# Optimization experiments

Measured on AMD Instinct MI355X. Metric: run time of the kernel, lower is better.

## Reference

```python
import jax, jax.numpy as jnp
import numpy as np

N = 100000      # nodes
E = 1600000     # edges per adjacency
NFEAT = 128
NHID = 128


def _digcn_conv(x, w, b, src, dst, edge_attr, num_nodes):
    # x @ W, then gather source, scale by edge weight, scatter-add to dst (PyG add-aggr)
    h = x @ w                                   # [N, out]
    msg = edge_attr[:, None] * h[src]           # [E, out]
    out = jax.ops.segment_sum(msg, dst, num_segments=num_nodes)
    return out + b


def _inception(x, ln_w, ln_b, c1_w, c1_b, c2_w, c2_b,
               edge_index, edge_attr, edge_index2, edge_attr2):
    x0 = x @ ln_w + ln_b
    x1 = _digcn_conv(x, c1_w, c1_b, edge_index[0], edge_index[1], edge_attr, x.shape[0])
    x2 = _digcn_conv(x, c2_w, c2_b, edge_index2[0], edge_index2[1], edge_attr2, x.shape[0])
    # eval mode: dropout is identity; the module sums the three branches
    return x0 + x1 + x2


def _mk_params(key, dims):
    ps = {}
    blocks = [("b1", NFEAT, NHID), ("b2", NHID, NHID), ("b3", NHID, NHID)]
    for name, din, dout in blocks:
        for pfx in ("ln", "c1", "c2"):
            key, k1 = jax.random.split(key)
            ps[f"{name}_{pfx}_w"] = jax.random.normal(k1, (din, dout), jnp.float32) * (1.0 / np.sqrt(din))
            ps[f"{name}_{pfx}_b"] = jnp.zeros((dout,), jnp.float32)
    return ps


def setup_inputs() -> dict:
    key = jax.random.key(0)
    ks = jax.random.split(key, 8)
    inp = {
        "x": jax.random.normal(ks[0], (N, NFEAT), jnp.float32),
        "edge_index": jax.random.randint(ks[1], (2, E), 0, N, jnp.int64 if jax.config.jax_enable_x64 else jnp.int32).astype(jnp.int32),
        "edge_attr": jax.random.uniform(ks[2], (E,), jnp.float32),
        "edge_index2": jax.random.randint(ks[3], (2, E), 0, N).astype(jnp.int32),
        "edge_attr2": jax.random.uniform(ks[4], (E,), jnp.float32),
    }
    inp.update(_mk_params(ks[5], None))
    return inp


def reference(x, edge_index, edge_attr, edge_index2, edge_attr2,
              b1_ln_w, b1_ln_b, b1_c1_w, b1_c1_b, b1_c2_w, b1_c2_b,
              b2_ln_w, b2_ln_b, b2_c1_w, b2_c1_b, b2_c2_w, b2_c2_b,
              b3_ln_w, b3_ln_b, b3_c1_w, b3_c1_b, b3_c2_w, b3_c2_b):
    x = _inception(x, b1_ln_w, b1_ln_b, b1_c1_w, b1_c1_b, b1_c2_w, b1_c2_b,
                   edge_index, edge_attr, edge_index2, edge_attr2)
    x = _inception(x, b2_ln_w, b2_ln_b, b2_c1_w, b2_c1_b, b2_c2_w, b2_c2_b,
                   edge_index, edge_attr, edge_index2, edge_attr2)
    x = _inception(x, b3_ln_w, b3_ln_b, b3_c1_w, b3_c1_b, b3_c2_w, b3_c2_b,
                   edge_index, edge_attr, edge_index2, edge_attr2)
    # torch module splits x per-graph via data.batch (data-dependent shapes);
    # we return the full node embedding matrix [N, NHID] instead.
    return x
```

## Files before the change

kernel.cpp:

```cpp
#include <hip/hip_runtime.h>

#define DIM 128
#define CHUNK 8192
#define NBK 256
#define BSHIFT 10

typedef __attribute__((ext_vector_type(8))) short bf16x8;
typedef __attribute__((ext_vector_type(4))) float f32x4;
typedef __attribute__((ext_vector_type(2))) unsigned u32x2;
typedef __attribute__((ext_vector_type(4))) unsigned u32x4;

static __device__ __forceinline__ short f2bf(float f) {
    union { float f; unsigned u; } v; v.f = f;
    unsigned r = (v.u + 0x7FFF + ((v.u >> 16) & 1)) >> 16;
    return (short)r;
}
static __device__ __forceinline__ float asf(unsigned u) {
    union { unsigned u; float f; } v; v.u = u; return v.f;
}
static __device__ __forceinline__ unsigned asu(float f) {
    union { float f; unsigned u; } v; v.f = f; return v.u;
}
static __device__ __forceinline__ unsigned pk2(float a, float b) {
    return (unsigned)(unsigned short)f2bf(a) | ((unsigned)(unsigned short)f2bf(b) << 16);
}

struct WPtrs { const float* w[9]; };
__global__ __launch_bounds__(256) void prep_w_k(WPtrs p, short* __restrict__ wt)
{
    const int g = blockIdx.x * 256 + threadIdx.x;
    if (g >= 3 * 12 * 8 * 64) return;
    const int lane = g & 63;
    const int ct   = (g >> 6) & 7;
    const int rest = g >> 9;
    const int ks   = rest % 12;
    const int layer = rest / 12;
    const int mat   = ks >> 2;
    const int n     = ct * 16 + (lane & 15);
    const int kbase = (ks & 3) * 32 + (lane >> 4) * 8;
    const float* W = p.w[layer * 3 + mat];
    short* dst = wt + (size_t)layer * 49152 + ks * 4096 + ct * 512 + lane * 8;
#pragma unroll
    for (int j = 0; j < 8; ++j) dst[j] = f2bf(W[(size_t)(kbase + j) * DIM + n]);
}

__global__ __launch_bounds__(256) void cast_k(
    const float* __restrict__ X, short* __restrict__ Xb, int n8)
{
    const int i = blockIdx.x * 256 + threadIdx.x;
    if (i >= n8) return;
    const float4* xp = (const float4*)X + (size_t)i * 2;
    const float4 a = xp[0];
    const float4 b = xp[1];
    bf16x8 v;
    v[0] = f2bf(a.x); v[1] = f2bf(a.y); v[2] = f2bf(a.z); v[3] = f2bf(a.w);
    v[4] = f2bf(b.x); v[5] = f2bf(b.y); v[6] = f2bf(b.z); v[7] = f2bf(b.w);
    *(bf16x8*)(Xb + (size_t)i * 8) = v;
}

__global__ __launch_bounds__(256) void mfma_gemm_k(
    const short* __restrict__ Xb, const short* __restrict__ G1,
    const short* __restrict__ G2, const short* __restrict__ Wp,
    const float* __restrict__ b0, const float* __restrict__ b1,
    const float* __restrict__ b2,
    float* __restrict__ Yf, short* __restrict__ Yb, int N)
{
    __shared__ __align__(16) short As[64][384 + 8];
    __shared__ __align__(16) short Bs[4096];
    const int t  = threadIdx.x;
    const int m0 = blockIdx.x * 64;

    for (int idx = t; idx < 64 * 48; idx += 256) {
        const int r = idx / 48;
        const int c = (idx % 48) * 8;
        bf16x8 v = (bf16x8){0,0,0,0,0,0,0,0};
        if (m0 + r < N) {
            if (c < 128)
                v = *(const bf16x8*)(Xb + (size_t)(m0 + r) * DIM + c);
            else if (c < 256)
                v = __builtin_nontemporal_load((const bf16x8*)(G1 + (size_t)(m0 + r) * DIM + (c - 128)));
            else
                v = __builtin_nontemporal_load((const bf16x8*)(G2 + (size_t)(m0 + r) * DIM + (c - 256)));
        }
        *(bf16x8*)&As[r][c] = v;
    }
    __syncthreads();

    const int wave  = t >> 6;
    const int lane  = t & 63;
    const int l15   = lane & 15;
    const int kq    = lane >> 4;
    const int mbase = wave * 16;

    bf16x8 afr[12];
#pragma unroll
    for (int ks = 0; ks < 12; ++ks)
        afr[ks] = *(const bf16x8*)&As[mbase + l15][ks * 32 + kq * 8];

    f32x4 acc[8];
#pragma unroll
    for (int ct = 0; ct < 8; ++ct) acc[ct] = (f32x4){0.f, 0.f, 0.f, 0.f};

#pragma unroll
    for (int ks = 0; ks < 12; ++ks) {
        if (ks) __syncthreads();
        const uint4* wsrc = (const uint4*)(Wp + ks * 4096);
        ((uint4*)Bs)[t]       = wsrc[t];
        ((uint4*)Bs)[t + 256] = wsrc[t + 256];
        __syncthreads();

        const bf16x8 a = afr[ks];
#pragma unroll
        for (int ct = 0; ct < 8; ++ct) {
            const bf16x8 b = *(const bf16x8*)&Bs[ct * 512 + lane * 8];
            acc[ct] = __builtin_amdgcn_mfma_f32_16x16x32_bf16(a, b, acc[ct], 0, 0, 0);
        }
    }

#pragma unroll
    for (int ct = 0; ct < 8; ++ct) {
        const int col = ct * 16 + l15;
        const float bias = b0[col] + b1[col] + b2[col];
#pragma unroll
        for (int r = 0; r < 4; ++r) {
            const int m = m0 + mbase + kq * 4 + r;
            if (m >= N) continue;
            const float v = acc[ct][r] + bias;
            if (Yf) __builtin_nontemporal_store(v, &Yf[(size_t)m * DIM + col]);
            else    Yb[(size_t)m * DIM + col] = f2bf(v);
        }
    }
}


__global__ __launch_bounds__(256) void p0_bhist_k(
    const int* __restrict__ d1, const int* __restrict__ d2,
    int* __restrict__ bcnt, int N, int E, int E2)
{
    __shared__ int lh[NBK];
    const int t = threadIdx.x;
    lh[t] = 0;
    __syncthreads();
    const int stride = gridDim.x * 256;
    for (int i = blockIdx.x * 256 + t; i < E;  i += stride) atomicAdd(&lh[d1[i] >> BSHIFT], 1);
    for (int i = blockIdx.x * 256 + t; i < E2; i += stride) atomicAdd(&lh[(N + d2[i]) >> BSHIFT], 1);
    __syncthreads();
    if (lh[t]) atomicAdd(&bcnt[t], lh[t]);
}

__global__ __launch_bounds__(256) void bscan_k(
    const int* __restrict__ bcnt, int* __restrict__ bktbase,
    int* __restrict__ cursor, int* __restrict__ rowptr, int twoN, int ET)
{
    __shared__ int sv[NBK];
    const int t = threadIdx.x;
    sv[t] = bcnt[t];
    __syncthreads();
    for (int off = 1; off < NBK; off <<= 1) {
        int a = (t >= off) ? sv[t - off] : 0;
        __syncthreads();
        sv[t] += a;
        __syncthreads();
    }
    const int excl = t ? sv[t - 1] : 0;
    bktbase[t] = excl;
    cursor[t]  = excl;
    if (t == 0) rowptr[twoN] = ET;
}

__global__ __launch_bounds__(256) void p1_bin_k(
    const int* __restrict__ s1, const int* __restrict__ d1, const float* __restrict__ ea1,
    const int* __restrict__ s2, const int* __restrict__ d2, const float* __restrict__ ea2,
    int* __restrict__ cursor, uint2* __restrict__ binned,
    int N, int E, int E2, int nc1)
{
    __shared__ __align__(16) uint2 stage[CHUNK];
    __shared__ unsigned char lbkt[CHUNK];
    __shared__ int hist[NBK], exclv[NBK], lcur[NBK], gpos[NBK];

    const int t = threadIdx.x;
    const int c = blockIdx.x;
    const bool a2 = (c >= nc1);
    const int* S  = a2 ? s2  : s1;
    const int* D  = a2 ? d2  : d1;
    const float* W = a2 ? ea2 : ea1;
    const int Eloc = a2 ? E2 : E;
    const int voff = a2 ? N : 0;
    const int eb   = (a2 ? (c - nc1) : c) * CHUNK;
    const int ec   = min(CHUNK, Eloc - eb);

    hist[t] = 0;
    __syncthreads();

    for (int i = t; i < ec; i += 256)
        atomicAdd(&hist[(unsigned)(voff + D[eb + i]) >> BSHIFT], 1);
    __syncthreads();

    exclv[t] = hist[t];
    __syncthreads();
    for (int off = 1; off < NBK; off <<= 1) {
        int a = (t >= off) ? exclv[t - off] : 0;
        __syncthreads();
        exclv[t] += a;
        __syncthreads();
    }
    const int myincl = exclv[t];
    __syncthreads();
    exclv[t] = myincl - hist[t];
    lcur[t]  = exclv[t];
    if (hist[t]) gpos[t] = atomicAdd(&cursor[t], hist[t]);
    __syncthreads();

    for (int i = t; i < ec; i += 256) {
        const int v = voff + D[eb + i];
        const int b = (unsigned)v >> BSHIFT;
        const int lpos = atomicAdd(&lcur[b], 1);
        stage[lpos] = make_uint2((unsigned)S[eb + i] | ((unsigned)(v & 1023) << 17),
                                 asu(W[eb + i]));
        lbkt[lpos] = (unsigned char)b;
    }
    __syncthreads();

    for (int s = t; s < ec; s += 256) {
        const int b = lbkt[s];
        binned[gpos[b] + (s - exclv[b])] = stage[s];
    }
}

__global__ __launch_bounds__(256) void p2_final_k(
    const uint2* __restrict__ binned, const int* __restrict__ bktbase,
    int* __restrict__ rowptr, uint2* __restrict__ pairs, int twoN)
{
    __shared__ int hist[1024], scn[1024], lcur[1024];
    const int t = threadIdx.x;
    const int b = blockIdx.x;
    const int base = bktbase[b];
    const int cnt  = bktbase[b + 1] - base;
    const int vbase = b << BSHIFT;

    for (int i = t; i < 1024; i += 256) hist[i] = 0;
    __syncthreads();

    for (int i = t; i < cnt; i += 256)
        atomicAdd(&hist[binned[base + i].x >> 17], 1);
    __syncthreads();

    for (int i = t; i < 1024; i += 256) scn[i] = hist[i];
    __syncthreads();
    for (int off = 1; off < 1024; off <<= 1) {
        int a0 = (t       >= off) ? scn[t       - off] : 0;
        int a1 = (t + 256 >= off) ? scn[t + 256 - off] : 0;
        int a2 = (t + 512 >= off) ? scn[t + 512 - off] : 0;
        int a3 = (t + 768 >= off) ? scn[t + 768 - off] : 0;
        __syncthreads();
        scn[t] += a0; scn[t + 256] += a1; scn[t + 512] += a2; scn[t + 768] += a3;
        __syncthreads();
    }
    for (int i = t; i < 1024; i += 256) {
        const int excl = scn[i] - hist[i];
        lcur[i] = excl;
        const int v = vbase + i;
        if (v < twoN) rowptr[v] = base + excl;
    }
    __syncthreads();

    for (int i = t; i < cnt; i += 256) {
        const uint2 e = binned[base + i];
        const int vlow = e.x >> 17;
        const int pos = base + atomicAdd(&lcur[vlow], 1);
        pairs[pos] = make_uint2(e.x & 0x1FFFFu, e.y);
    }
}


static __device__ __forceinline__ void bf2acc8(unsigned w, u32x4 h, float* acc)
{
    const float wf = asf(w);
    acc[0] = fmaf(wf, asf(h.x << 16),         acc[0]);
    acc[1] = fmaf(wf, asf(h.x & 0xFFFF0000u), acc[1]);
    acc[2] = fmaf(wf, asf(h.y << 16),         acc[2]);
    acc[3] = fmaf(wf, asf(h.y & 0xFFFF0000u), acc[3]);
    acc[4] = fmaf(wf, asf(h.z << 16),         acc[4]);
    acc[5] = fmaf(wf, asf(h.z & 0xFFFF0000u), acc[5]);
    acc[6] = fmaf(wf, asf(h.w << 16),         acc[6]);
    acc[7] = fmaf(wf, asf(h.w & 0xFFFF0000u), acc[7]);
}

static __device__ __forceinline__ void gacc16(
    const short* __restrict__ H, const uint2* __restrict__ pairs,
    int start, int end, int s, float* acc)
{
    int j = start;
    for (; j + 7 < end; j += 8) {
        u32x2 p[8]; u32x4 h[8];
#pragma unroll
        for (int q = 0; q < 8; ++q)
            p[q] = __builtin_nontemporal_load((const u32x2*)(pairs + j + q));
#pragma unroll
        for (int q = 0; q < 8; ++q)
            h[q] = *(const u32x4*)(H + (size_t)p[q].x * DIM + s * 8);
#pragma unroll
        for (int q = 0; q < 8; ++q) bf2acc8(p[q].y, h[q], acc);
    }
    if (j + 3 < end) {
        u32x2 p[4]; u32x4 h[4];
#pragma unroll
        for (int q = 0; q < 4; ++q)
            p[q] = __builtin_nontemporal_load((const u32x2*)(pairs + j + q));
#pragma unroll
        for (int q = 0; q < 4; ++q)
            h[q] = *(const u32x4*)(H + (size_t)p[q].x * DIM + s * 8);
#pragma unroll
        for (int q = 0; q < 4; ++q) bf2acc8(p[q].y, h[q], acc);
        j += 4;
    }
    for (; j < end; ++j) {
        const u32x2 p = __builtin_nontemporal_load((const u32x2*)(pairs + j));
        const u32x4 h = *(const u32x4*)(H + (size_t)p.x * DIM + s * 8);
        bf2acc8(p.y, h, acc);
    }
}

__global__ __launch_bounds__(256) void gatherX_k(
    const short* __restrict__ Xb,
    const uint2* __restrict__ pairs, const int* __restrict__ rowptr,
    short* __restrict__ G1, short* __restrict__ G2, int N)
{
    const int node = blockIdx.x * 16 + (threadIdx.x >> 4);
    if (node >= N) return;
    const int s = threadIdx.x & 15;

    const int s1 = rowptr[node];
    const int e1 = rowptr[node + 1];
    const int s2 = rowptr[N + node];
    const int e2 = rowptr[N + node + 1];

    float a1[8] = {0.f, 0.f, 0.f, 0.f, 0.f, 0.f, 0.f, 0.f};
    float a2[8] = {0.f, 0.f, 0.f, 0.f, 0.f, 0.f, 0.f, 0.f};
    gacc16(Xb, pairs, s1, e1, s, a1);
    gacc16(Xb, pairs, s2, e2, s, a2);

    const size_t off = (size_t)node * DIM + s * 8;
    u32x4 o1 = (u32x4){pk2(a1[0], a1[1]), pk2(a1[2], a1[3]),
                       pk2(a1[4], a1[5]), pk2(a1[6], a1[7])};
    u32x4 o2 = (u32x4){pk2(a2[0], a2[1]), pk2(a2[2], a2[3]),
                       pk2(a2[4], a2[5]), pk2(a2[6], a2[7])};
    __builtin_nontemporal_store(o1, (u32x4*)(G1 + off));
    __builtin_nontemporal_store(o2, (u32x4*)(G2 + off));
}

extern "C" void kernel_launch(void* const* d_in, const int* in_sizes, int n_in,
                              void* d_out, int out_size, void* d_ws, size_t ws_size,
                              hipStream_t stream)
{
    const float* x   = (const float*)d_in[0];
    const int*   ei  = (const int*)d_in[1];
    const float* ea  = (const float*)d_in[2];
    const int*   ei2 = (const int*)d_in[3];
    const float* ea2 = (const float*)d_in[4];

    const int N  = in_sizes[0] / DIM;
    const int E  = in_sizes[2];
    const int E2 = in_sizes[4];
    const int ET = E + E2;

    float* OUT = (float*)d_out;

    short* Xb0 = (short*)d_ws;
    short* Xb1 = Xb0 + (size_t)N * DIM;
    short* G1  = Xb1 + (size_t)N * DIM;
    short* G2  = G1  + (size_t)N * DIM;
    short* WT  = G2  + (size_t)N * DIM;
    int*   rowptr = (int*)(WT + 3 * 49152);
    int*   bcnt   = rowptr + 2 * N + 4;
    int*   bktbase= bcnt + NBK;
    int*   cursor = bktbase + NBK + 4;
    uint2* pairs  = (uint2*)(cursor + NBK);
    uint2* binned = (uint2*)G1;

    WPtrs wp;
    for (int b = 0; b < 3; ++b) {
        wp.w[b * 3 + 0] = (const float*)d_in[5 + 6 * b + 0];
        wp.w[b * 3 + 1] = (const float*)d_in[5 + 6 * b + 2];
        wp.w[b * 3 + 2] = (const float*)d_in[5 + 6 * b + 4];
    }
    prep_w_k<<<(18432 + 255) / 256, 256, 0, stream>>>(wp, WT);

    const int n8 = N * DIM / 8;
    cast_k<<<(n8 + 255) / 256, 256, 0, stream>>>(x, Xb0, n8);

    const int nc1 = (E + CHUNK - 1) / CHUNK;
    const int nc2 = (E2 + CHUNK - 1) / CHUNK;
    const int nbk_used = (2 * N + (1 << BSHIFT) - 1) >> BSHIFT;

    hipMemsetAsync(bcnt, 0, NBK * sizeof(int), stream);
    p0_bhist_k<<<256, 256, 0, stream>>>(ei + E, ei2 + E2, bcnt, N, E, E2);
    bscan_k<<<1, NBK, 0, stream>>>(bcnt, bktbase, cursor, rowptr, 2 * N, ET);
    p1_bin_k<<<nc1 + nc2, 256, 0, stream>>>(ei, ei + E, ea, ei2, ei2 + E2, ea2,
                                            cursor, binned, N, E, E2, nc1);
    p2_final_k<<<nbk_used, 256, 0, stream>>>(binned, bktbase, rowptr, pairs, 2 * N);

    const int gGemm   = (N + 63) / 64;
    const int gGather = (N + 15) / 16;

    const short* cur = Xb0;
    for (int b = 0; b < 3; ++b) {
        const float* lnb = (const float*)d_in[5 + 6 * b + 1];
        const float* c1b = (const float*)d_in[5 + 6 * b + 3];
        const float* c2b = (const float*)d_in[5 + 6 * b + 5];

        gatherX_k<<<gGather, 256, 0, stream>>>(cur, pairs, rowptr, G1, G2, N);

        float* yf = (b == 2) ? OUT : nullptr;
        short* yb = (b == 2) ? nullptr : ((cur == Xb0) ? Xb1 : Xb0);

        mfma_gemm_k<<<gGemm, 256, 0, stream>>>(
            cur, G1, G2, WT + (size_t)b * 49152, lnb, c1b, c2b, yf, yb, N);

        if (b < 2) cur = yb;
    }
}
```

Measured before the change: 838.4 us.

## Fuse edge gather-aggregation with MFMA GEMM into one per-layer kernel

Merges the gather kernel and the GEMM kernel so each block aggregates neighbour features for its 64 nodes straight into shared memory and then runs the MFMA projection. This removes the G1/G2 intermediate write and readback through global memory and cuts one launch per layer. The x-part and weight fragments now load directly from global memory (L2-cached) instead of being staged in LDS, so the per-k-step syncs go away. The cost is that the irregular gather and the MFMA work now share one block, which can lower occupancy and hide latency less well.

```diff
diff --git a/kernel.cpp b/kernel.cpp
--- a/kernel.cpp
+++ b/kernel.cpp
@@ -58,80 +58,6 @@
     *(bf16x8*)(Xb + (size_t)i * 8) = v;
 }
 
-__global__ __launch_bounds__(256) void mfma_gemm_k(
-    const short* __restrict__ Xb, const short* __restrict__ G1,
-    const short* __restrict__ G2, const short* __restrict__ Wp,
-    const float* __restrict__ b0, const float* __restrict__ b1,
-    const float* __restrict__ b2,
-    float* __restrict__ Yf, short* __restrict__ Yb, int N)
-{
-    __shared__ __align__(16) short As[64][384 + 8];
-    __shared__ __align__(16) short Bs[4096];
-    const int t  = threadIdx.x;
-    const int m0 = blockIdx.x * 64;
-
-    for (int idx = t; idx < 64 * 48; idx += 256) {
-        const int r = idx / 48;
-        const int c = (idx % 48) * 8;
-        bf16x8 v = (bf16x8){0,0,0,0,0,0,0,0};
-        if (m0 + r < N) {
-            if (c < 128)
-                v = *(const bf16x8*)(Xb + (size_t)(m0 + r) * DIM + c);
-            else if (c < 256)
-                v = __builtin_nontemporal_load((const bf16x8*)(G1 + (size_t)(m0 + r) * DIM + (c - 128)));
-            else
-                v = __builtin_nontemporal_load((const bf16x8*)(G2 + (size_t)(m0 + r) * DIM + (c - 256)));
-        }
-        *(bf16x8*)&As[r][c] = v;
-    }
-    __syncthreads();
-
-    const int wave  = t >> 6;
-    const int lane  = t & 63;
-    const int l15   = lane & 15;
-    const int kq    = lane >> 4;
-    const int mbase = wave * 16;
-
-    bf16x8 afr[12];
-#pragma unroll
-    for (int ks = 0; ks < 12; ++ks)
-        afr[ks] = *(const bf16x8*)&As[mbase + l15][ks * 32 + kq * 8];
-
-    f32x4 acc[8];
-#pragma unroll
-    for (int ct = 0; ct < 8; ++ct) acc[ct] = (f32x4){0.f, 0.f, 0.f, 0.f};
-
-#pragma unroll
-    for (int ks = 0; ks < 12; ++ks) {
-        if (ks) __syncthreads();
-        const uint4* wsrc = (const uint4*)(Wp + ks * 4096);
-        ((uint4*)Bs)[t]       = wsrc[t];
-        ((uint4*)Bs)[t + 256] = wsrc[t + 256];
-        __syncthreads();
-
-        const bf16x8 a = afr[ks];
-#pragma unroll
-        for (int ct = 0; ct < 8; ++ct) {
-            const bf16x8 b = *(const bf16x8*)&Bs[ct * 512 + lane * 8];
-            acc[ct] = __builtin_amdgcn_mfma_f32_16x16x32_bf16(a, b, acc[ct], 0, 0, 0);
-        }
-    }
-
-#pragma unroll
-    for (int ct = 0; ct < 8; ++ct) {
-        const int col = ct * 16 + l15;
-        const float bias = b0[col] + b1[col] + b2[col];
-#pragma unroll
-        for (int r = 0; r < 4; ++r) {
-            const int m = m0 + mbase + kq * 4 + r;
-            if (m >= N) continue;
-            const float v = acc[ct][r] + bias;
-            if (Yf) __builtin_nontemporal_store(v, &Yf[(size_t)m * DIM + col]);
-            else    Yb[(size_t)m * DIM + col] = f2bf(v);
-        }
-    }
-}
-
 
 __global__ __launch_bounds__(256) void p0_bhist_k(
     const int* __restrict__ d1, const int* __restrict__ d2,
@@ -272,7 +198,6 @@
     }
 }
 
-
 static __device__ __forceinline__ void bf2acc8(unsigned w, u32x4 h, float* acc)
 {
     const float wf = asf(w);
@@ -321,32 +246,83 @@
     }
 }
 
-__global__ __launch_bounds__(256) void gatherX_k(
-    const short* __restrict__ Xb,
+__global__ __launch_bounds__(256, 4) void fused_layer_k(
+    const short* __restrict__ Xb, const short* __restrict__ Wp,
     const uint2* __restrict__ pairs, const int* __restrict__ rowptr,
-    short* __restrict__ G1, short* __restrict__ G2, int N)
-{
-    const int node = blockIdx.x * 16 + (threadIdx.x >> 4);
-    if (node >= N) return;
-    const int s = threadIdx.x & 15;
-
-    const int s1 = rowptr[node];
-    const int e1 = rowptr[node + 1];
-    const int s2 = rowptr[N + node];
-    const int e2 = rowptr[N + node + 1];
-
-    float a1[8] = {0.f, 0.f, 0.f, 0.f, 0.f, 0.f, 0.f, 0.f};
-    float a2[8] = {0.f, 0.f, 0.f, 0.f, 0.f, 0.f, 0.f, 0.f};
-    gacc16(Xb, pairs, s1, e1, s, a1);
-    gacc16(Xb, pairs, s2, e2, s, a2);
-
-    const size_t off = (size_t)node * DIM + s * 8;
-    u32x4 o1 = (u32x4){pk2(a1[0], a1[1]), pk2(a1[2], a1[3]),
-                       pk2(a1[4], a1[5]), pk2(a1[6], a1[7])};
-    u32x4 o2 = (u32x4){pk2(a2[0], a2[1]), pk2(a2[2], a2[3]),
-                       pk2(a2[4], a2[5]), pk2(a2[6], a2[7])};
-    __builtin_nontemporal_store(o1, (u32x4*)(G1 + off));
-    __builtin_nontemporal_store(o2, (u32x4*)(G2 + off));
+    const float* __restrict__ b0, const float* __restrict__ b1,
+    const float* __restrict__ b2,
+    float* __restrict__ Yf, short* __restrict__ Yb, int N)
+{
+    __shared__ __align__(16) short As[64][272];
+    const int t  = threadIdx.x;
+    const int m0 = blockIdx.x * 64;
+
+    const int s    = t & 15;
+    const int nrow = t >> 4;
+#pragma unroll
+    for (int nl = 0; nl < 4; ++nl) {
+        const int r    = nl * 16 + nrow;
+        const int node = m0 + r;
+        float a1[8] = {0.f,0.f,0.f,0.f,0.f,0.f,0.f,0.f};
+        float a2[8] = {0.f,0.f,0.f,0.f,0.f,0.f,0.f,0.f};
+        if (node < N) {
+            gacc16(Xb, pairs, rowptr[node],     rowptr[node + 1],     s, a1);
+            gacc16(Xb, pairs, rowptr[N + node], rowptr[N + node + 1], s, a2);
+        }
+        u32x4 o1 = (u32x4){pk2(a1[0], a1[1]), pk2(a1[2], a1[3]),
+                           pk2(a1[4], a1[5]), pk2(a1[6], a1[7])};
+        u32x4 o2 = (u32x4){pk2(a2[0], a2[1]), pk2(a2[2], a2[3]),
+                           pk2(a2[4], a2[5]), pk2(a2[6], a2[7])};
+        *(u32x4*)&As[r][s * 8]       = o1;
+        *(u32x4*)&As[r][128 + s * 8] = o2;
+    }
+    __syncthreads();
+
+    const int wave  = t >> 6;
+    const int lane  = t & 63;
+    const int l15   = lane & 15;
+    const int kq    = lane >> 4;
+    const int mbase = wave * 16;
+    const int mrow  = m0 + mbase + l15;
+    const int mclmp = (mrow < N) ? mrow : (N - 1);
+    const short* xrow = Xb + (size_t)mclmp * DIM + kq * 8;
+
+    f32x4 acc[8];
+#pragma unroll
+    for (int ct = 0; ct < 8; ++ct) acc[ct] = (f32x4){0.f, 0.f, 0.f, 0.f};
+
+#pragma unroll
+    for (int ks = 0; ks < 4; ++ks) {
+        const bf16x8 a = *(const bf16x8*)(xrow + ks * 32);
+        const short* wb = Wp + ks * 4096 + lane * 8;
+#pragma unroll
+        for (int ct = 0; ct < 8; ++ct)
+            acc[ct] = __builtin_amdgcn_mfma_f32_16x16x32_bf16(
+                a, *(const bf16x8*)(wb + ct * 512), acc[ct], 0, 0, 0);
+    }
+#pragma unroll
+    for (int ks = 4; ks < 12; ++ks) {
+        const bf16x8 a = *(const bf16x8*)&As[mbase + l15][(ks - 4) * 32 + kq * 8];
+        const short* wb = Wp + ks * 4096 + lane * 8;
+#pragma unroll
+        for (int ct = 0; ct < 8; ++ct)
+            acc[ct] = __builtin_amdgcn_mfma_f32_16x16x32_bf16(
+                a, *(const bf16x8*)(wb + ct * 512), acc[ct], 0, 0, 0);
+    }
+
+#pragma unroll
+    for (int ct = 0; ct < 8; ++ct) {
+        const int col = ct * 16 + l15;
+        const float bias = b0[col] + b1[col] + b2[col];
+#pragma unroll
+        for (int r = 0; r < 4; ++r) {
+            const int m = m0 + mbase + kq * 4 + r;
+            if (m >= N) continue;
+            const float v = acc[ct][r] + bias;
+            if (Yf) __builtin_nontemporal_store(v, &Yf[(size_t)m * DIM + col]);
+            else    Yb[(size_t)m * DIM + col] = f2bf(v);
+        }
+    }
 }
 
 extern "C" void kernel_launch(void* const* d_in, const int* in_sizes, int n_in,
@@ -368,15 +344,13 @@
 
     short* Xb0 = (short*)d_ws;
     short* Xb1 = Xb0 + (size_t)N * DIM;
-    short* G1  = Xb1 + (size_t)N * DIM;
-    short* G2  = G1  + (size_t)N * DIM;
-    short* WT  = G2  + (size_t)N * DIM;
+    short* WT  = Xb1 + (size_t)N * DIM;
     int*   rowptr = (int*)(WT + 3 * 49152);
     int*   bcnt   = rowptr + 2 * N + 4;
     int*   bktbase= bcnt + NBK;
     int*   cursor = bktbase + NBK + 4;
     uint2* pairs  = (uint2*)(cursor + NBK);
-    uint2* binned = (uint2*)G1;
+    uint2* binned = pairs + ET;
 
     WPtrs wp;
     for (int b = 0; b < 3; ++b) {
@@ -400,8 +374,7 @@
                                             cursor, binned, N, E, E2, nc1);
     p2_final_k<<<nbk_used, 256, 0, stream>>>(binned, bktbase, rowptr, pairs, 2 * N);
 
-    const int gGemm   = (N + 63) / 64;
-    const int gGather = (N + 15) / 16;
+    const int gGemm = (N + 63) / 64;
 
     const short* cur = Xb0;
     for (int b = 0; b < 3; ++b) {
@@ -409,13 +382,11 @@
         const float* c1b = (const float*)d_in[5 + 6 * b + 3];
         const float* c2b = (const float*)d_in[5 + 6 * b + 5];
 
-        gatherX_k<<<gGather, 256, 0, stream>>>(cur, pairs, rowptr, G1, G2, N);
-
         float* yf = (b == 2) ? OUT : nullptr;
         short* yb = (b == 2) ? nullptr : ((cur == Xb0) ? Xb1 : Xb0);
 
-        mfma_gemm_k<<<gGemm, 256, 0, stream>>>(
-            cur, G1, G2, WT + (size_t)b * 49152, lnb, c1b, c2b, yf, yb, N);
+        fused_layer_k<<<gGemm, 256, 0, stream>>>(
+            cur, WT + (size_t)b * 49152, pairs, rowptr, lnb, c1b, c2b, yf, yb, N);
 
         if (b < 2) cur = yb;
     }
```

After: 785.1 us. 1.07x faster.
